# Optimization experiments

Hardware: AMD Instinct MI355X
Metric: run time of the kernel (lower is better)

## Reference

```python
import jax, jax.numpy as jnp
import numpy as np
from jax import lax

NUM_HEADS = 4
SIDE = 5  # side_dwconv


def setup_inputs() -> dict:
    key = jax.random.key(0)
    ks = jax.random.split(key, 7)
    B, C, H, W = 2, 128, 56, 56
    return {
        "x": jax.random.normal(ks[0], (B, C, H, W), dtype=jnp.float32),
        "qkv_w": jax.random.normal(ks[1], (3 * C, C), dtype=jnp.float32) * 0.02,
        "qkv_b": jax.random.normal(ks[2], (3 * C,), dtype=jnp.float32) * 0.02,
        "lepe_w": jax.random.normal(ks[3], (C, 1, SIDE, SIDE), dtype=jnp.float32) * 0.02,
        "lepe_b": jax.random.normal(ks[4], (C,), dtype=jnp.float32) * 0.02,
        "proj_w": jax.random.normal(ks[5], (C, C), dtype=jnp.float32) * 0.02,
        "proj_b": jax.random.normal(ks[6], (C,), dtype=jnp.float32) * 0.02,
    }


def reference(x, qkv_w, qkv_b, lepe_w, lepe_b, proj_w, proj_b):
    B, C, H, W = x.shape
    nh = NUM_HEADS
    hd = C // nh
    scale = hd ** (-0.5)
    N = H * W

    # 1x1 conv qkv == channel matmul
    qkv = jnp.einsum('oc,bchw->bohw', qkv_w, x) + qkv_b[None, :, None, None]
    q, k, v = jnp.split(qkv, 3, axis=1)  # each [B, C, H, W]

    qr = q.reshape(B, nh, hd, N)
    kr = k.reshape(B, nh, hd, N)
    vr = v.reshape(B, nh, hd, N)

    # attn = q^T k over head_dim -> [B, nh, N, N]
    attn = jnp.einsum('bhdn,bhdm->bhnm', qr, kr) * scale
    attn = jax.nn.softmax(attn, axis=-1)

    # out = attn @ v^T, then permute back to [B, C, H, W]
    out = jnp.einsum('bhnm,bhdm->bhdn', attn, vr).reshape(B, C, H, W)

    # depthwise LePE conv on v, fused with residual add
    pad = SIDE // 2
    lepe = lax.conv_general_dilated(
        v, lepe_w, window_strides=(1, 1), padding=[(pad, pad), (pad, pad)],
        dimension_numbers=('NCHW', 'OIHW', 'NCHW'), feature_group_count=C,
    ) + lepe_b[None, :, None, None]
    out = out + lepe

    # 1x1 conv proj
    out = jnp.einsum('oc,bchw->bohw', proj_w, out) + proj_b[None, :, None, None]
    return out
```

## Files before the change

### kernel.cpp

```cpp
#include <hip/hip_runtime.h>

typedef __bf16 bf16x8 __attribute__((ext_vector_type(8)));
typedef __bf16 bf16x4 __attribute__((ext_vector_type(4)));
typedef __bf16 bf16x2 __attribute__((ext_vector_type(2)));
typedef float  f32x4  __attribute__((ext_vector_type(4)));

#define NPIX  3136
#define WIMG  56
#define CCH   128
#define NH    4
#define HD    32
#define NSPLIT 8
#define QSCALE 0.2550565470841439f

#if __has_builtin(__builtin_amdgcn_exp2f)
#define FEXP2(x) __builtin_amdgcn_exp2f(x)
#else
#define FEXP2(x) __expf((x) * 0.6931471805599453f)
#endif


__global__ __launch_bounds__(256) void k_qkv(
    const float* __restrict__ x, const float* __restrict__ qkv_w,
    const float* __restrict__ qkv_b,
    __bf16* __restrict__ qT, __bf16* __restrict__ kT,
    __bf16* __restrict__ vT, __bf16* __restrict__ vP)
{
    __shared__ __bf16 xl[64][136];
    const int tid = threadIdx.x;
    const int w = tid >> 6, lane = tid & 63;
    const int col = lane & 15, g = lane >> 4;
    const int px0 = blockIdx.x * 64;
    const int oslab = blockIdx.y;
    const int b = blockIdx.z;
    const int obase = oslab * 64 + w * 16;

    {
        const int px = tid & 63, cq = tid >> 6;
        const float* xp = x + (size_t)b * CCH * NPIX + px0 + px;
        #pragma unroll
        for (int i = 0; i < 8; ++i) {
            const int c0 = cq * 4 + i * 16;
            const float v0 = xp[(size_t)(c0 + 0) * NPIX];
            const float v1 = xp[(size_t)(c0 + 1) * NPIX];
            const float v2 = xp[(size_t)(c0 + 2) * NPIX];
            const float v3 = xp[(size_t)(c0 + 3) * NPIX];
            bf16x4 bv = {(__bf16)v0, (__bf16)v1, (__bf16)v2, (__bf16)v3};
            *(bf16x4*)&xl[px][c0] = bv;
        }
    }
    __syncthreads();

    f32x4 acc[4];
    #pragma unroll
    for (int a = 0; a < 4; ++a) acc[a] = (f32x4){0.f, 0.f, 0.f, 0.f};

    const float* wrow = qkv_w + (size_t)(obase + col) * CCH;
    #pragma unroll
    for (int ks = 0; ks < 4; ++ks) {
        const int c0 = ks * 32 + g * 8;
        const float4 wA = *(const float4*)(wrow + c0);
        const float4 wB = *(const float4*)(wrow + c0 + 4);
        bf16x8 af = {(__bf16)wA.x, (__bf16)wA.y, (__bf16)wA.z, (__bf16)wA.w,
                     (__bf16)wB.x, (__bf16)wB.y, (__bf16)wB.z, (__bf16)wB.w};
        #pragma unroll
        for (int a = 0; a < 4; ++a) {
            const bf16x8 bf_ = *(const bf16x8*)&xl[16 * a + col][c0];
            acc[a] = __builtin_amdgcn_mfma_f32_16x16x32_bf16(af, bf_, acc[a], 0, 0, 0);
        }
    }

    const int orow = obase + g * 4;
    const f32x4 bias4 = *(const f32x4*)(qkv_b + orow);

    if (oslab < 2) {
        const int h = orow >> 5, d0 = orow & 31;
        __bf16* dst = qT + ((size_t)(b * NH + h) * NPIX) * HD + d0;
        #pragma unroll
        for (int a = 0; a < 4; ++a) {
            const int px = px0 + 16 * a + col;
            bf16x4 v;
            #pragma unroll
            for (int r = 0; r < 4; ++r) v[r] = (__bf16)((acc[a][r] + bias4[r]) * QSCALE);
            *(bf16x4*)(dst + (size_t)px * HD) = v;
        }
    } else if (oslab < 4) {
        const int o2 = orow - 128;
        const int h = o2 >> 5, d0 = o2 & 31;
        __bf16* dst = kT + ((size_t)(b * NH + h) * NPIX) * HD + d0;
        #pragma unroll
        for (int a = 0; a < 4; ++a) {
            const int px = px0 + 16 * a + col;
            bf16x4 v;
            #pragma unroll
            for (int r = 0; r < 4; ++r) v[r] = (__bf16)(acc[a][r] + bias4[r]);
            *(bf16x4*)(dst + (size_t)px * HD) = v;
        }
    } else {
        const int c = orow - 256;
        #pragma unroll
        for (int a = 0; a < 4; ++a) {
            const int px = px0 + 16 * a + col;
            bf16x4 v;
            #pragma unroll
            for (int r = 0; r < 4; ++r) v[r] = (__bf16)(acc[a][r] + bias4[r]);
            *(bf16x4*)(vT + ((size_t)(b * NPIX + px)) * CCH + c) = v;
            const int sp = px0 + 4 * col + a;
            #pragma unroll
            for (int r = 0; r < 4; ++r)
                vP[((size_t)(b * CCH + c + r)) * NPIX + sp] = v[r];
        }
    }
}

__global__ __launch_bounds__(64, 4) void k_attn(
    const __bf16* __restrict__ qT, const __bf16* __restrict__ kT,
    const __bf16* __restrict__ vP,
    __bf16* __restrict__ pO, float* __restrict__ pl)
{
    __shared__ __bf16 P[32][72];
    const int lane = threadIdx.x;
    const int col = lane & 15, g = lane >> 4;
    const int qt = blockIdx.x, bh = blockIdx.y, sp = blockIdx.z;
    const int b = bh >> 2, h = bh & 3;
    const int qbase = qt * 32;
    const size_t headoff = (size_t)bh * NPIX * HD;
    const int c0h = h * HD;

    const bf16x8 aqA = *(const bf16x8*)(qT + headoff + (size_t)(qbase + col) * HD + g * 8);
    const bf16x8 aqB = *(const bf16x8*)(qT + headoff + (size_t)(qbase + 16 + col) * HD + g * 8);

    const __bf16 one = (__bf16)1.0f;
    const bf16x8 ones = {one, one, one, one, one, one, one, one};

    f32x4 O[2][2], Lacc[2];
    #pragma unroll
    for (int i = 0; i < 2; ++i) {
        Lacc[i] = (f32x4){0.f, 0.f, 0.f, 0.f};
        #pragma unroll
        for (int j = 0; j < 2; ++j) O[i][j] = (f32x4){0.f, 0.f, 0.f, 0.f};
    }

    const __bf16* kTh   = kT + headoff;
    const __bf16* vrow0 = vP + (size_t)(b * CCH + c0h + col)      * NPIX;
    const __bf16* vrow1 = vP + (size_t)(b * CCH + c0h + 16 + col) * NPIX;

    const int cs = (49 * sp) >> 3, ce = (49 * (sp + 1)) >> 3;

#define LOADK(DK, KK) do { const int _k0 = (KK);                                          \
        _Pragma("unroll")                                                                 \
        for (int _c = 0; _c < 4; ++_c)                                                    \
            DK[_c] = *(const bf16x8*)(kTh + (size_t)(_k0 + 16 * _c + col) * HD + g * 8);  \
        } while (0)

    auto compute = [&](const bf16x8* bk, int k0) {
        const bf16x8 bv0 = *(const bf16x8*)(vrow0 + k0      + g * 8);
        const bf16x8 bv1 = *(const bf16x8*)(vrow0 + k0 + 32 + g * 8);
        const bf16x8 bv2 = *(const bf16x8*)(vrow1 + k0      + g * 8);
        const bf16x8 bv3 = *(const bf16x8*)(vrow1 + k0 + 32 + g * 8);
        const f32x4 z = {0.f, 0.f, 0.f, 0.f};
        #pragma unroll
        for (int qh = 0; qh < 2; ++qh) {
            const bf16x8 aq = qh ? aqB : aqA;
            f32x4 s0 = __builtin_amdgcn_mfma_f32_16x16x32_bf16(aq, bk[0], z, 0, 0, 0);
            f32x4 s1 = __builtin_amdgcn_mfma_f32_16x16x32_bf16(aq, bk[1], z, 0, 0, 0);
            f32x4 s2 = __builtin_amdgcn_mfma_f32_16x16x32_bf16(aq, bk[2], z, 0, 0, 0);
            f32x4 s3 = __builtin_amdgcn_mfma_f32_16x16x32_bf16(aq, bk[3], z, 0, 0, 0);
            #pragma unroll
            for (int r = 0; r < 4; ++r) {
                bf16x4 pv = {(__bf16)FEXP2(s0[r]), (__bf16)FEXP2(s1[r]),
                             (__bf16)FEXP2(s2[r]), (__bf16)FEXP2(s3[r])};
                *(bf16x4*)&P[qh * 16 + g * 4 + r][4 * col] = pv;
            }
        }
        #pragma unroll
        for (int qh = 0; qh < 2; ++qh) {
            const bf16x8 ap0 = *(const bf16x8*)&P[qh * 16 + col][g * 8];
            const bf16x8 ap1 = *(const bf16x8*)&P[qh * 16 + col][32 + g * 8];
            O[qh][0] = __builtin_amdgcn_mfma_f32_16x16x32_bf16(ap0, bv0, O[qh][0], 0, 0, 0);
            O[qh][0] = __builtin_amdgcn_mfma_f32_16x16x32_bf16(ap1, bv1, O[qh][0], 0, 0, 0);
            O[qh][1] = __builtin_amdgcn_mfma_f32_16x16x32_bf16(ap0, bv2, O[qh][1], 0, 0, 0);
            O[qh][1] = __builtin_amdgcn_mfma_f32_16x16x32_bf16(ap1, bv3, O[qh][1], 0, 0, 0);
            Lacc[qh] = __builtin_amdgcn_mfma_f32_16x16x32_bf16(ap0, ones, Lacc[qh], 0, 0, 0);
            Lacc[qh] = __builtin_amdgcn_mfma_f32_16x16x32_bf16(ap1, ones, Lacc[qh], 0, 0, 0);
        }
    };

    bf16x8 kA[4], kB[4];
    LOADK(kA, cs * 64);
    int cc = cs;
    while (cc + 2 <= ce) {
        LOADK(kB, (cc + 1) * 64);
        compute(kA, cc * 64);
        LOADK(kA, ((cc + 2 < ce) ? cc + 2 : cs) * 64);
        compute(kB, (cc + 1) * 64);
        cc += 2;
    }
    if (cc < ce) compute(kA, cc * 64);
#undef LOADK

    const int t = bh * 98 + qt;
    __bf16* po = pO + ((size_t)t * NSPLIT + sp) * 1024;
    #pragma unroll
    for (int qh = 0; qh < 2; ++qh)
        #pragma unroll
        for (int dh = 0; dh < 2; ++dh) {
            bf16x4 v = {(__bf16)O[qh][dh][0], (__bf16)O[qh][dh][1],
                        (__bf16)O[qh][dh][2], (__bf16)O[qh][dh][3]};
            *(bf16x4*)(po + (dh * 16 + col) * 32 + qh * 16 + g * 4) = v;
        }
    if (col == 0) {
        float* plp = pl + ((size_t)t * NSPLIT + sp) * 32;
        *(f32x4*)(plp + g * 4)      = Lacc[0];
        *(f32x4*)(plp + 16 + g * 4) = Lacc[1];
    }
}

__global__ __launch_bounds__(256) void k_reduce(
    const __bf16* __restrict__ pO, const float* __restrict__ pl,
    const __bf16* __restrict__ vT,
    const float* __restrict__ lepe_w, const float* __restrict__ lepe_b,
    __bf16* __restrict__ attnT)
{
    __shared__ float wl[32][25];
    __shared__ float bl[32];
    const int tid = threadIdx.x;
    const int qt = blockIdx.x, bh = blockIdx.y;
    const int b = bh >> 2, h = bh & 3;
    const int c0h = h * HD;

    for (int i = tid; i < 800; i += 256) ((float*)wl)[i] = lepe_w[c0h * 25 + i];
    if (tid < 32) bl[tid] = lepe_b[c0h + tid];
    __syncthreads();

    const int q = tid >> 3;
    const int cq = (tid & 7) * 4;
    const int t = bh * 98 + qt;

    float lt = 0.f;
    float o[4] = {0.f, 0.f, 0.f, 0.f};
    #pragma unroll
    for (int s = 0; s < NSPLIT; ++s) {
        lt += pl[((size_t)t * NSPLIT + s) * 32 + q];
        const __bf16* base = pO + ((size_t)t * NSPLIT + s) * 1024 + q;
        #pragma unroll
        for (int i = 0; i < 4; ++i) o[i] += (float)base[(cq + i) * 32];
    }
    const float linv = 1.0f / lt;
    #pragma unroll
    for (int i = 0; i < 4; ++i) o[i] = o[i] * linv + bl[cq + i];

    const int px = qt * 32 + q;
    const int py = px / WIMG, pxx = px % WIMG;
    const __bf16* vtb = vT + ((size_t)b * NPIX) * CCH + c0h + cq;
    #pragma unroll
    for (int dy = 0; dy < 5; ++dy) {
        const int yy = py + dy - 2;
        if (yy < 0 || yy >= WIMG) continue;
        #pragma unroll
        for (int dx = 0; dx < 5; ++dx) {
            const int xx = pxx + dx - 2;
            if (xx < 0 || xx >= WIMG) continue;
            const bf16x4 vv = *(const bf16x4*)(vtb + (size_t)(yy * WIMG + xx) * CCH);
            const int tap = dy * 5 + dx;
            #pragma unroll
            for (int i = 0; i < 4; ++i) o[i] += (float)vv[i] * wl[cq + i][tap];
        }
    }
    bf16x4 ov = {(__bf16)o[0], (__bf16)o[1], (__bf16)o[2], (__bf16)o[3]};
    *(bf16x4*)(attnT + ((size_t)(b * NPIX + px)) * CCH + c0h + cq) = ov;
}

__global__ __launch_bounds__(256) void k_proj(
    const __bf16* __restrict__ attnT, const float* __restrict__ proj_w,
    const float* __restrict__ proj_b, float* __restrict__ out)
{
    const int tid = threadIdx.x;
    const int w = tid >> 6, lane = tid & 63;
    const int col = lane & 15, g = lane >> 4;
    const int px0 = blockIdx.x * 32 + (w >> 1) * 16;
    const int obase = blockIdx.y * 32 + (w & 1) * 16;
    const int b = blockIdx.z;

    const float* wrow = proj_w + (size_t)(obase + col) * CCH;
    const __bf16* abase = attnT + (size_t)(b * NPIX + px0) * CCH;

    f32x4 acc = {0.f, 0.f, 0.f, 0.f};
    #pragma unroll
    for (int ks = 0; ks < 4; ++ks) {
        const int c0 = ks * 32 + g * 8;
        const float4 wA = *(const float4*)(wrow + c0);
        const float4 wB = *(const float4*)(wrow + c0 + 4);
        bf16x8 af = {(__bf16)wA.x, (__bf16)wA.y, (__bf16)wA.z, (__bf16)wA.w,
                     (__bf16)wB.x, (__bf16)wB.y, (__bf16)wB.z, (__bf16)wB.w};
        const bf16x8 bf_ = *(const bf16x8*)(abase + (size_t)col * CCH + c0);
        acc = __builtin_amdgcn_mfma_f32_16x16x32_bf16(af, bf_, acc, 0, 0, 0);
    }

    const f32x4 pb = *(const f32x4*)(proj_b + obase + g * 4);
    #pragma unroll
    for (int r = 0; r < 4; ++r)
        out[(size_t)(b * CCH + obase + g * 4 + r) * NPIX + px0 + col] = acc[r] + pb[r];
}

extern "C" void kernel_launch(void* const* d_in, const int* in_sizes, int n_in,
                              void* d_out, int out_size, void* d_ws, size_t ws_size,
                              hipStream_t stream)
{
    const float* x      = (const float*)d_in[0];
    const float* qkv_w  = (const float*)d_in[1];
    const float* qkv_b  = (const float*)d_in[2];
    const float* lepe_w = (const float*)d_in[3];
    const float* lepe_b = (const float*)d_in[4];
    const float* proj_w = (const float*)d_in[5];
    const float* proj_b = (const float*)d_in[6];
    float* out = (float*)d_out;

    char* p = (char*)d_ws;
    __bf16* qT    = (__bf16*)p;  p += (size_t)2 * NH * NPIX * HD * 2;
    __bf16* kT    = (__bf16*)p;  p += (size_t)2 * NH * NPIX * HD * 2;
    __bf16* vT    = (__bf16*)p;  p += (size_t)2 * NPIX * CCH * 2;
    __bf16* vP    = (__bf16*)p;  p += (size_t)2 * CCH * NPIX * 2;
    __bf16* attnT = (__bf16*)p;  p += (size_t)2 * NPIX * CCH * 2;
    __bf16* pO    = (__bf16*)p;  p += (size_t)784 * NSPLIT * 1024 * 2;
    float*  pl    = (float*)p;

    k_qkv   <<<dim3(49, 6, 2), dim3(256), 0, stream>>>(x, qkv_w, qkv_b, qT, kT, vT, vP);
    k_attn  <<<dim3(98, 8, NSPLIT), dim3(64), 0, stream>>>(qT, kT, vP, pO, pl);
    k_reduce<<<dim3(98, 8),    dim3(256), 0, stream>>>(pO, pl, vT, lepe_w, lepe_b, attnT);
    k_proj  <<<dim3(98, 4, 2), dim3(256), 0, stream>>>(attnT, proj_w, proj_b, out);
}
```

Before: 136.1 us.

## Fuse reduce and proj kernels, widen qkv tiles, pack two attention waves per block

```diff
diff --git a/kernel.cpp b/kernel.cpp
--- a/kernel.cpp
+++ b/kernel.cpp
@@ -2,7 +2,6 @@
 
 typedef __bf16 bf16x8 __attribute__((ext_vector_type(8)));
 typedef __bf16 bf16x4 __attribute__((ext_vector_type(4)));
-typedef __bf16 bf16x2 __attribute__((ext_vector_type(2)));
 typedef float  f32x4  __attribute__((ext_vector_type(4)));
 
 #define NPIX  3136
@@ -31,9 +30,9 @@
     const int w = tid >> 6, lane = tid & 63;
     const int col = lane & 15, g = lane >> 4;
     const int px0 = blockIdx.x * 64;
-    const int oslab = blockIdx.y;
+    const int slab = blockIdx.y;
     const int b = blockIdx.z;
-    const int obase = oslab * 64 + w * 16;
+    const int obase = slab * 128 + w * 32;
 
     {
         const int px = tid & 63, cq = tid >> 6;
@@ -51,77 +50,85 @@
     }
     __syncthreads();
 
-    f32x4 acc[4];
-    #pragma unroll
-    for (int a = 0; a < 4; ++a) acc[a] = (f32x4){0.f, 0.f, 0.f, 0.f};
-
-    const float* wrow = qkv_w + (size_t)(obase + col) * CCH;
+    f32x4 acc[2][4];
+    #pragma unroll
+    for (int ot = 0; ot < 2; ++ot)
+        #pragma unroll
+        for (int a = 0; a < 4; ++a) acc[ot][a] = (f32x4){0.f, 0.f, 0.f, 0.f};
+
     #pragma unroll
     for (int ks = 0; ks < 4; ++ks) {
         const int c0 = ks * 32 + g * 8;
-        const float4 wA = *(const float4*)(wrow + c0);
-        const float4 wB = *(const float4*)(wrow + c0 + 4);
-        bf16x8 af = {(__bf16)wA.x, (__bf16)wA.y, (__bf16)wA.z, (__bf16)wA.w,
-                     (__bf16)wB.x, (__bf16)wB.y, (__bf16)wB.z, (__bf16)wB.w};
-        #pragma unroll
-        for (int a = 0; a < 4; ++a) {
-            const bf16x8 bf_ = *(const bf16x8*)&xl[16 * a + col][c0];
-            acc[a] = __builtin_amdgcn_mfma_f32_16x16x32_bf16(af, bf_, acc[a], 0, 0, 0);
-        }
-    }
-
-    const int orow = obase + g * 4;
-    const f32x4 bias4 = *(const f32x4*)(qkv_b + orow);
-
-    if (oslab < 2) {
-        const int h = orow >> 5, d0 = orow & 31;
-        __bf16* dst = qT + ((size_t)(b * NH + h) * NPIX) * HD + d0;
-        #pragma unroll
-        for (int a = 0; a < 4; ++a) {
-            const int px = px0 + 16 * a + col;
-            bf16x4 v;
-            #pragma unroll
-            for (int r = 0; r < 4; ++r) v[r] = (__bf16)((acc[a][r] + bias4[r]) * QSCALE);
-            *(bf16x4*)(dst + (size_t)px * HD) = v;
-        }
-    } else if (oslab < 4) {
-        const int o2 = orow - 128;
-        const int h = o2 >> 5, d0 = o2 & 31;
-        __bf16* dst = kT + ((size_t)(b * NH + h) * NPIX) * HD + d0;
-        #pragma unroll
-        for (int a = 0; a < 4; ++a) {
-            const int px = px0 + 16 * a + col;
-            bf16x4 v;
-            #pragma unroll
-            for (int r = 0; r < 4; ++r) v[r] = (__bf16)(acc[a][r] + bias4[r]);
-            *(bf16x4*)(dst + (size_t)px * HD) = v;
-        }
-    } else {
-        const int c = orow - 256;
-        #pragma unroll
-        for (int a = 0; a < 4; ++a) {
-            const int px = px0 + 16 * a + col;
-            bf16x4 v;
-            #pragma unroll
-            for (int r = 0; r < 4; ++r) v[r] = (__bf16)(acc[a][r] + bias4[r]);
-            *(bf16x4*)(vT + ((size_t)(b * NPIX + px)) * CCH + c) = v;
-            const int sp = px0 + 4 * col + a;
-            #pragma unroll
-            for (int r = 0; r < 4; ++r)
-                vP[((size_t)(b * CCH + c + r)) * NPIX + sp] = v[r];
+        #pragma unroll
+        for (int ot = 0; ot < 2; ++ot) {
+            const float* wrow = qkv_w + (size_t)(obase + ot * 16 + col) * CCH + c0;
+            const float4 wA = *(const float4*)(wrow);
+            const float4 wB = *(const float4*)(wrow + 4);
+            bf16x8 af = {(__bf16)wA.x, (__bf16)wA.y, (__bf16)wA.z, (__bf16)wA.w,
+                         (__bf16)wB.x, (__bf16)wB.y, (__bf16)wB.z, (__bf16)wB.w};
+            #pragma unroll
+            for (int a = 0; a < 4; ++a) {
+                const bf16x8 bf_ = *(const bf16x8*)&xl[16 * a + col][c0];
+                acc[ot][a] = __builtin_amdgcn_mfma_f32_16x16x32_bf16(af, bf_, acc[ot][a], 0, 0, 0);
+            }
+        }
+    }
+
+    #pragma unroll
+    for (int ot = 0; ot < 2; ++ot) {
+        const int orow = obase + ot * 16 + g * 4;
+        const f32x4 bias4 = *(const f32x4*)(qkv_b + orow);
+        if (slab == 0) {
+            const int o = orow, h = o >> 5, d0 = o & 31;
+            __bf16* dst = qT + ((size_t)(b * NH + h) * NPIX) * HD + d0;
+            #pragma unroll
+            for (int a = 0; a < 4; ++a) {
+                const int px = px0 + 16 * a + col;
+                bf16x4 v;
+                #pragma unroll
+                for (int r = 0; r < 4; ++r) v[r] = (__bf16)((acc[ot][a][r] + bias4[r]) * QSCALE);
+                *(bf16x4*)(dst + (size_t)px * HD) = v;
+            }
+        } else if (slab == 1) {
+            const int o = orow - 128, h = o >> 5, d0 = o & 31;
+            __bf16* dst = kT + ((size_t)(b * NH + h) * NPIX) * HD + d0;
+            #pragma unroll
+            for (int a = 0; a < 4; ++a) {
+                const int px = px0 + 16 * a + col;
+                bf16x4 v;
+                #pragma unroll
+                for (int r = 0; r < 4; ++r) v[r] = (__bf16)(acc[ot][a][r] + bias4[r]);
+                *(bf16x4*)(dst + (size_t)px * HD) = v;
+            }
+        } else {
+            const int c = orow - 256;
+            #pragma unroll
+            for (int a = 0; a < 4; ++a) {
+                const int px = px0 + 16 * a + col;
+                bf16x4 v;
+                #pragma unroll
+                for (int r = 0; r < 4; ++r) v[r] = (__bf16)(acc[ot][a][r] + bias4[r]);
+                *(bf16x4*)(vT + ((size_t)(b * NPIX + px)) * CCH + c) = v;
+                const int sp = px0 + 4 * col + a;
+                #pragma unroll
+                for (int r = 0; r < 4; ++r)
+                    vP[((size_t)(b * CCH + c + r)) * NPIX + sp] = v[r];
+            }
         }
     }
 }
 
-__global__ __launch_bounds__(64, 4) void k_attn(
+__global__ __launch_bounds__(128) void k_attn(
     const __bf16* __restrict__ qT, const __bf16* __restrict__ kT,
     const __bf16* __restrict__ vP,
     __bf16* __restrict__ pO, float* __restrict__ pl)
 {
-    __shared__ __bf16 P[32][72];
-    const int lane = threadIdx.x;
+    __shared__ __bf16 P[2][32][72];
+    const int tid = threadIdx.x;
+    const int w = tid >> 6, lane = tid & 63;
     const int col = lane & 15, g = lane >> 4;
-    const int qt = blockIdx.x, bh = blockIdx.y, sp = blockIdx.z;
+    const int qt = blockIdx.x * 2 + w;
+    const int bh = blockIdx.y, sp = blockIdx.z;
     const int b = bh >> 2, h = bh & 3;
     const int qbase = qt * 32;
     const size_t headoff = (size_t)bh * NPIX * HD;
@@ -147,13 +154,12 @@
 
     const int cs = (49 * sp) >> 3, ce = (49 * (sp + 1)) >> 3;
 
-#define LOADK(DK, KK) do { const int _k0 = (KK);                                          \
-        _Pragma("unroll")                                                                 \
-        for (int _c = 0; _c < 4; ++_c)                                                    \
-            DK[_c] = *(const bf16x8*)(kTh + (size_t)(_k0 + 16 * _c + col) * HD + g * 8);  \
-        } while (0)
-
-    auto compute = [&](const bf16x8* bk, int k0) {
+    for (int cc = cs; cc < ce; ++cc) {
+        const int k0 = cc * 64;
+        bf16x8 bk0 = *(const bf16x8*)(kTh + (size_t)(k0      + col) * HD + g * 8);
+        bf16x8 bk1 = *(const bf16x8*)(kTh + (size_t)(k0 + 16 + col) * HD + g * 8);
+        bf16x8 bk2 = *(const bf16x8*)(kTh + (size_t)(k0 + 32 + col) * HD + g * 8);
+        bf16x8 bk3 = *(const bf16x8*)(kTh + (size_t)(k0 + 48 + col) * HD + g * 8);
         const bf16x8 bv0 = *(const bf16x8*)(vrow0 + k0      + g * 8);
         const bf16x8 bv1 = *(const bf16x8*)(vrow0 + k0 + 32 + g * 8);
         const bf16x8 bv2 = *(const bf16x8*)(vrow1 + k0      + g * 8);
@@ -162,21 +168,21 @@
         #pragma unroll
         for (int qh = 0; qh < 2; ++qh) {
             const bf16x8 aq = qh ? aqB : aqA;
-            f32x4 s0 = __builtin_amdgcn_mfma_f32_16x16x32_bf16(aq, bk[0], z, 0, 0, 0);
-            f32x4 s1 = __builtin_amdgcn_mfma_f32_16x16x32_bf16(aq, bk[1], z, 0, 0, 0);
-            f32x4 s2 = __builtin_amdgcn_mfma_f32_16x16x32_bf16(aq, bk[2], z, 0, 0, 0);
-            f32x4 s3 = __builtin_amdgcn_mfma_f32_16x16x32_bf16(aq, bk[3], z, 0, 0, 0);
+            f32x4 s0 = __builtin_amdgcn_mfma_f32_16x16x32_bf16(aq, bk0, z, 0, 0, 0);
+            f32x4 s1 = __builtin_amdgcn_mfma_f32_16x16x32_bf16(aq, bk1, z, 0, 0, 0);
+            f32x4 s2 = __builtin_amdgcn_mfma_f32_16x16x32_bf16(aq, bk2, z, 0, 0, 0);
+            f32x4 s3 = __builtin_amdgcn_mfma_f32_16x16x32_bf16(aq, bk3, z, 0, 0, 0);
             #pragma unroll
             for (int r = 0; r < 4; ++r) {
                 bf16x4 pv = {(__bf16)FEXP2(s0[r]), (__bf16)FEXP2(s1[r]),
                              (__bf16)FEXP2(s2[r]), (__bf16)FEXP2(s3[r])};
-                *(bf16x4*)&P[qh * 16 + g * 4 + r][4 * col] = pv;
+                *(bf16x4*)&P[w][qh * 16 + g * 4 + r][4 * col] = pv;
             }
         }
         #pragma unroll
         for (int qh = 0; qh < 2; ++qh) {
-            const bf16x8 ap0 = *(const bf16x8*)&P[qh * 16 + col][g * 8];
-            const bf16x8 ap1 = *(const bf16x8*)&P[qh * 16 + col][32 + g * 8];
+            const bf16x8 ap0 = *(const bf16x8*)&P[w][qh * 16 + col][g * 8];
+            const bf16x8 ap1 = *(const bf16x8*)&P[w][qh * 16 + col][32 + g * 8];
             O[qh][0] = __builtin_amdgcn_mfma_f32_16x16x32_bf16(ap0, bv0, O[qh][0], 0, 0, 0);
             O[qh][0] = __builtin_amdgcn_mfma_f32_16x16x32_bf16(ap1, bv1, O[qh][0], 0, 0, 0);
             O[qh][1] = __builtin_amdgcn_mfma_f32_16x16x32_bf16(ap0, bv2, O[qh][1], 0, 0, 0);
@@ -184,31 +190,17 @@
             Lacc[qh] = __builtin_amdgcn_mfma_f32_16x16x32_bf16(ap0, ones, Lacc[qh], 0, 0, 0);
             Lacc[qh] = __builtin_amdgcn_mfma_f32_16x16x32_bf16(ap1, ones, Lacc[qh], 0, 0, 0);
         }
-    };
-
-    bf16x8 kA[4], kB[4];
-    LOADK(kA, cs * 64);
-    int cc = cs;
-    while (cc + 2 <= ce) {
-        LOADK(kB, (cc + 1) * 64);
-        compute(kA, cc * 64);
-        LOADK(kA, ((cc + 2 < ce) ? cc + 2 : cs) * 64);
-        compute(kB, (cc + 1) * 64);
-        cc += 2;
-    }
-    if (cc < ce) compute(kA, cc * 64);
-#undef LOADK
+    }
 
     const int t = bh * 98 + qt;
     __bf16* po = pO + ((size_t)t * NSPLIT + sp) * 1024;
     #pragma unroll
     for (int qh = 0; qh < 2; ++qh)
         #pragma unroll
-        for (int dh = 0; dh < 2; ++dh) {
-            bf16x4 v = {(__bf16)O[qh][dh][0], (__bf16)O[qh][dh][1],
-                        (__bf16)O[qh][dh][2], (__bf16)O[qh][dh][3]};
-            *(bf16x4*)(po + (dh * 16 + col) * 32 + qh * 16 + g * 4) = v;
-        }
+        for (int dh = 0; dh < 2; ++dh)
+            #pragma unroll
+            for (int r = 0; r < 4; ++r)
+                po[(qh * 16 + g * 4 + r) * 32 + dh * 16 + col] = (__bf16)O[qh][dh][r];
     if (col == 0) {
         float* plp = pl + ((size_t)t * NSPLIT + sp) * 32;
         *(f32x4*)(plp + g * 4)      = Lacc[0];
@@ -216,91 +208,96 @@
     }
 }
 
-__global__ __launch_bounds__(256) void k_reduce(
+__global__ __launch_bounds__(256) void k_rproj(
     const __bf16* __restrict__ pO, const float* __restrict__ pl,
     const __bf16* __restrict__ vT,
     const float* __restrict__ lepe_w, const float* __restrict__ lepe_b,
-    __bf16* __restrict__ attnT)
+    const float* __restrict__ proj_w, const float* __restrict__ proj_b,
+    float* __restrict__ out)
 {
-    __shared__ float wl[32][25];
-    __shared__ float bl[32];
+    __shared__ __bf16 at[32][136];
+    __shared__ float  wl[CCH][25];
+    __shared__ float  bl[CCH];
     const int tid = threadIdx.x;
-    const int qt = blockIdx.x, bh = blockIdx.y;
-    const int b = bh >> 2, h = bh & 3;
-    const int c0h = h * HD;
-
-    for (int i = tid; i < 800; i += 256) ((float*)wl)[i] = lepe_w[c0h * 25 + i];
-    if (tid < 32) bl[tid] = lepe_b[c0h + tid];
+    const int qt = blockIdx.x, b = blockIdx.y;
+
+    for (int i = tid; i < CCH * 25; i += 256) ((float*)wl)[i] = lepe_w[i];
+    if (tid < CCH) bl[tid] = lepe_b[tid];
     __syncthreads();
 
-    const int q = tid >> 3;
-    const int cq = (tid & 7) * 4;
-    const int t = bh * 98 + qt;
-
-    float lt = 0.f;
-    float o[4] = {0.f, 0.f, 0.f, 0.f};
-    #pragma unroll
-    for (int s = 0; s < NSPLIT; ++s) {
-        lt += pl[((size_t)t * NSPLIT + s) * 32 + q];
-        const __bf16* base = pO + ((size_t)t * NSPLIT + s) * 1024 + q;
-        #pragma unroll
-        for (int i = 0; i < 4; ++i) o[i] += (float)base[(cq + i) * 32];
-    }
-    const float linv = 1.0f / lt;
-    #pragma unroll
-    for (int i = 0; i < 4; ++i) o[i] = o[i] * linv + bl[cq + i];
-
-    const int px = qt * 32 + q;
-    const int py = px / WIMG, pxx = px % WIMG;
-    const __bf16* vtb = vT + ((size_t)b * NPIX) * CCH + c0h + cq;
-    #pragma unroll
-    for (int dy = 0; dy < 5; ++dy) {
-        const int yy = py + dy - 2;
-        if (yy < 0 || yy >= WIMG) continue;
-        #pragma unroll
-        for (int dx = 0; dx < 5; ++dx) {
-            const int xx = pxx + dx - 2;
-            if (xx < 0 || xx >= WIMG) continue;
-            const bf16x4 vv = *(const bf16x4*)(vtb + (size_t)(yy * WIMG + xx) * CCH);
-            const int tap = dy * 5 + dx;
-            #pragma unroll
-            for (int i = 0; i < 4; ++i) o[i] += (float)vv[i] * wl[cq + i][tap];
-        }
-    }
-    bf16x4 ov = {(__bf16)o[0], (__bf16)o[1], (__bf16)o[2], (__bf16)o[3]};
-    *(bf16x4*)(attnT + ((size_t)(b * NPIX + px)) * CCH + c0h + cq) = ov;
-}
-
-__global__ __launch_bounds__(256) void k_proj(
-    const __bf16* __restrict__ attnT, const float* __restrict__ proj_w,
-    const float* __restrict__ proj_b, float* __restrict__ out)
-{
-    const int tid = threadIdx.x;
+    const int q   = tid >> 3;
+    const int cq4 = (tid & 7) * 4;
+    const int px  = qt * 32 + q;
+    const int py  = px / WIMG, pxx = px % WIMG;
+
+    #pragma unroll
+    for (int h = 0; h < NH; ++h) {
+        const int c = h * HD + cq4;
+        const size_t t = (size_t)(b * NH + h) * 98 + qt;
+        float lt = 0.f;
+        float o[4] = {0.f, 0.f, 0.f, 0.f};
+        #pragma unroll
+        for (int s = 0; s < NSPLIT; ++s) {
+            lt += pl[(t * NSPLIT + s) * 32 + q];
+            const bf16x4 pv = *(const bf16x4*)(pO + (t * NSPLIT + s) * 1024 + q * 32 + cq4);
+            #pragma unroll
+            for (int i = 0; i < 4; ++i) o[i] += (float)pv[i];
+        }
+        const float linv = 1.0f / lt;
+        #pragma unroll
+        for (int i = 0; i < 4; ++i) o[i] = o[i] * linv + bl[c + i];
+
+        const __bf16* vtb = vT + ((size_t)b * NPIX) * CCH + c;
+        #pragma unroll
+        for (int dy = 0; dy < 5; ++dy) {
+            const int yy = py + dy - 2;
+            if (yy < 0 || yy >= WIMG) continue;
+            #pragma unroll
+            for (int dx = 0; dx < 5; ++dx) {
+                const int xx = pxx + dx - 2;
+                if (xx < 0 || xx >= WIMG) continue;
+                const bf16x4 vv = *(const bf16x4*)(vtb + (size_t)(yy * WIMG + xx) * CCH);
+                const int tap = dy * 5 + dx;
+                #pragma unroll
+                for (int i = 0; i < 4; ++i) o[i] += (float)vv[i] * wl[c + i][tap];
+            }
+        }
+        bf16x4 ov = {(__bf16)o[0], (__bf16)o[1], (__bf16)o[2], (__bf16)o[3]};
+        *(bf16x4*)&at[q][c] = ov;
+    }
+    __syncthreads();
+
     const int w = tid >> 6, lane = tid & 63;
     const int col = lane & 15, g = lane >> 4;
-    const int px0 = blockIdx.x * 32 + (w >> 1) * 16;
-    const int obase = blockIdx.y * 32 + (w & 1) * 16;
-    const int b = blockIdx.z;
-
-    const float* wrow = proj_w + (size_t)(obase + col) * CCH;
-    const __bf16* abase = attnT + (size_t)(b * NPIX + px0) * CCH;
-
-    f32x4 acc = {0.f, 0.f, 0.f, 0.f};
-    #pragma unroll
-    for (int ks = 0; ks < 4; ++ks) {
-        const int c0 = ks * 32 + g * 8;
-        const float4 wA = *(const float4*)(wrow + c0);
-        const float4 wB = *(const float4*)(wrow + c0 + 4);
-        bf16x8 af = {(__bf16)wA.x, (__bf16)wA.y, (__bf16)wA.z, (__bf16)wA.w,
-                     (__bf16)wB.x, (__bf16)wB.y, (__bf16)wB.z, (__bf16)wB.w};
-        const bf16x8 bf_ = *(const bf16x8*)(abase + (size_t)col * CCH + c0);
-        acc = __builtin_amdgcn_mfma_f32_16x16x32_bf16(af, bf_, acc, 0, 0, 0);
-    }
-
-    const f32x4 pb = *(const f32x4*)(proj_b + obase + g * 4);
-    #pragma unroll
-    for (int r = 0; r < 4; ++r)
-        out[(size_t)(b * CCH + obase + g * 4 + r) * NPIX + px0 + col] = acc[r] + pb[r];
+    const int obase = w * 32;
+
+    #pragma unroll
+    for (int ot = 0; ot < 2; ++ot) {
+        const float* wrow = proj_w + (size_t)(obase + ot * 16 + col) * CCH;
+        f32x4 acc[2];
+        acc[0] = (f32x4){0.f, 0.f, 0.f, 0.f};
+        acc[1] = (f32x4){0.f, 0.f, 0.f, 0.f};
+        #pragma unroll
+        for (int ks = 0; ks < 4; ++ks) {
+            const int c0 = ks * 32 + g * 8;
+            const float4 wA = *(const float4*)(wrow + c0);
+            const float4 wB = *(const float4*)(wrow + c0 + 4);
+            bf16x8 af = {(__bf16)wA.x, (__bf16)wA.y, (__bf16)wA.z, (__bf16)wA.w,
+                         (__bf16)wB.x, (__bf16)wB.y, (__bf16)wB.z, (__bf16)wB.w};
+            #pragma unroll
+            for (int a = 0; a < 2; ++a) {
+                const bf16x8 bf_ = *(const bf16x8*)&at[16 * a + col][c0];
+                acc[a] = __builtin_amdgcn_mfma_f32_16x16x32_bf16(af, bf_, acc[a], 0, 0, 0);
+            }
+        }
+        const f32x4 pb = *(const f32x4*)(proj_b + obase + ot * 16 + g * 4);
+        #pragma unroll
+        for (int a = 0; a < 2; ++a)
+            #pragma unroll
+            for (int r = 0; r < 4; ++r)
+                out[(size_t)(b * CCH + obase + ot * 16 + g * 4 + r) * NPIX
+                    + qt * 32 + 16 * a + col] = acc[a][r] + pb[r];
+    }
 }
 
 extern "C" void kernel_launch(void* const* d_in, const int* in_sizes, int n_in,
@@ -317,16 +314,15 @@
     float* out = (float*)d_out;
 
     char* p = (char*)d_ws;
-    __bf16* qT    = (__bf16*)p;  p += (size_t)2 * NH * NPIX * HD * 2;
-    __bf16* kT    = (__bf16*)p;  p += (size_t)2 * NH * NPIX * HD * 2;
-    __bf16* vT    = (__bf16*)p;  p += (size_t)2 * NPIX * CCH * 2;
-    __bf16* vP    = (__bf16*)p;  p += (size_t)2 * CCH * NPIX * 2;
-    __bf16* attnT = (__bf16*)p;  p += (size_t)2 * NPIX * CCH * 2;
-    __bf16* pO    = (__bf16*)p;  p += (size_t)784 * NSPLIT * 1024 * 2;
-    float*  pl    = (float*)p;
-
-    k_qkv   <<<dim3(49, 6, 2), dim3(256), 0, stream>>>(x, qkv_w, qkv_b, qT, kT, vT, vP);
-    k_attn  <<<dim3(98, 8, NSPLIT), dim3(64), 0, stream>>>(qT, kT, vP, pO, pl);
-    k_reduce<<<dim3(98, 8),    dim3(256), 0, stream>>>(pO, pl, vT, lepe_w, lepe_b, attnT);
-    k_proj  <<<dim3(98, 4, 2), dim3(256), 0, stream>>>(attnT, proj_w, proj_b, out);
+    __bf16* qT = (__bf16*)p;  p += (size_t)2 * NH * NPIX * HD * 2;
+    __bf16* kT = (__bf16*)p;  p += (size_t)2 * NH * NPIX * HD * 2;
+    __bf16* vT = (__bf16*)p;  p += (size_t)2 * NPIX * CCH * 2;
+    __bf16* vP = (__bf16*)p;  p += (size_t)2 * CCH * NPIX * 2;
+    __bf16* pO = (__bf16*)p;  p += (size_t)784 * NSPLIT * 1024 * 2;
+    float*  pl = (float*)p;
+
+    k_qkv  <<<dim3(49, 3, 2),      dim3(256), 0, stream>>>(x, qkv_w, qkv_b, qT, kT, vT, vP);
+    k_attn <<<dim3(49, 8, NSPLIT), dim3(128), 0, stream>>>(qT, kT, vP, pO, pl);
+    k_rproj<<<dim3(98, 2),         dim3(256), 0, stream>>>(pO, pl, vT, lepe_w, lepe_b,
+                                                           proj_w, proj_b, out);
 }
```

After: 142.3 us. 4.5% more time.
